# Kernel optimization log

Hardware: AMD Instinct MI355X
Metric: run time of the kernel (lower is better)

## Reference

```python
import jax, jax.numpy as jnp
import numpy as np
import math

D_MODEL = 1024
NUM_HEADS = 16
D_K = D_MODEL // NUM_HEADS
B, T = 2, 2048


def setup_inputs() -> dict:
    key = jax.random.key(0)
    ks = jax.random.split(key, 9)
    s = 1.0 / math.sqrt(D_MODEL)
    inp = {
        'x': jax.random.normal(ks[0], (B, T, D_MODEL), dtype=jnp.float32),
        'mask': jnp.tril(jnp.ones((1, 1, T, T), dtype=jnp.int32)),
        'Wq': jax.random.uniform(ks[1], (D_MODEL, D_MODEL), jnp.float32, -s, s),
        'bq': jax.random.uniform(ks[2], (D_MODEL,), jnp.float32, -s, s),
        'Wk': jax.random.uniform(ks[3], (D_MODEL, D_MODEL), jnp.float32, -s, s),
        'bk': jax.random.uniform(ks[4], (D_MODEL,), jnp.float32, -s, s),
        'Wv': jax.random.uniform(ks[5], (D_MODEL, D_MODEL), jnp.float32, -s, s),
        'bv': jax.random.uniform(ks[6], (D_MODEL,), jnp.float32, -s, s),
        'Wo': jax.random.uniform(ks[7], (D_MODEL, D_MODEL), jnp.float32, -s, s),
        'bo': jax.random.uniform(ks[8], (D_MODEL,), jnp.float32, -s, s),
    }
    return inp


def reference(x, mask, Wq, bq, Wk, bk, Wv, bv, Wo, bo):
    Bsz, Tlen, C = x.shape
    # projections; torch Linear computes x @ W.T + b, here W stored as (in,out)-like square so use x @ W + b with W meaning W.T
    q = (x @ Wq + bq).reshape(Bsz, Tlen, NUM_HEADS, D_K).transpose(0, 2, 1, 3)
    k = (x @ Wk + bk).reshape(Bsz, Tlen, NUM_HEADS, D_K).transpose(0, 2, 1, 3)
    v = (x @ Wv + bv).reshape(Bsz, Tlen, NUM_HEADS, D_K).transpose(0, 2, 1, 3)
    scores = jnp.einsum('bhqd,bhkd->bhqk', q, k) / math.sqrt(D_K)  # (B,H,T,T)
    scores = jnp.where(mask == 0, -jnp.inf, scores)
    attn = jax.nn.softmax(scores, axis=-1)
    out = jnp.einsum('bhqk,bhkd->bhqd', attn, v)
    out = out.transpose(0, 2, 1, 3).reshape(Bsz, Tlen, C)
    return out @ Wo + bo
```

## Files before the change

### kernel.cpp

```cpp
#include <hip/hip_runtime.h>
#include <math.h>

typedef unsigned short ushort_t;
typedef short short8 __attribute__((ext_vector_type(8)));
typedef float f32x4 __attribute__((ext_vector_type(4)));

#define DMODEL 1024
#define NHEADS 16
#define DKH    64
#define BATCH  2
#define SEQ    2048
#define BT     (BATCH * SEQ)

__device__ __forceinline__ ushort_t f2bf(float f) {
    union { float f; unsigned u; } a; a.f = f;
    return (ushort_t)((a.u + 0x7FFFu + ((a.u >> 16) & 1u)) >> 16);
}

__device__ __forceinline__ void async_copy16(const ushort_t* g, ushort_t* l) {
    __builtin_amdgcn_global_load_lds(
        (__attribute__((address_space(1))) void*)g,
        (__attribute__((address_space(3))) void*)l, 16, 0, 0);
}

__global__ __launch_bounds__(256) void cast_x_kernel(
    const float* __restrict__ x, ushort_t* __restrict__ xb)
{
    size_t i = ((size_t)blockIdx.x * 256 + threadIdx.x) * 8;
    float4 a = *(const float4*)(x + i);
    float4 b = *(const float4*)(x + i + 4);
    union { ushort_t u[8]; short8 v; } r;
    r.u[0] = f2bf(a.x); r.u[1] = f2bf(a.y); r.u[2] = f2bf(a.z); r.u[3] = f2bf(a.w);
    r.u[4] = f2bf(b.x); r.u[5] = f2bf(b.y); r.u[6] = f2bf(b.z); r.u[7] = f2bf(b.w);
    *(short8*)(xb + i) = r.v;
}

__global__ __launch_bounds__(256) void wtrans_kernel(
    const float* __restrict__ Wq, const float* __restrict__ Wk,
    const float* __restrict__ Wv, const float* __restrict__ Wo,
    ushort_t* __restrict__ WqT, ushort_t* __restrict__ WkT,
    ushort_t* __restrict__ WvT, ushort_t* __restrict__ WoT)
{
    const int z = blockIdx.z;
    const float* W = (z == 0) ? Wq : (z == 1) ? Wk : (z == 2) ? Wv : Wo;
    ushort_t*   WT = (z == 0) ? WqT : (z == 1) ? WkT : (z == 2) ? WvT : WoT;

    __shared__ ushort_t tile[64][72];
    const int k0 = blockIdx.x * 64, n0 = blockIdx.y * 64;
    const int tid = threadIdx.x;

    const int r  = tid >> 2;
    const int cb = (tid & 3) * 16;
#pragma unroll
    for (int u = 0; u < 4; ++u) {
        float4 v = *(const float4*)(W + (size_t)(k0 + r) * DMODEL + n0 + cb + u * 4);
        union { ushort_t u4[4]; unsigned long long ll; } p;
        p.u4[0] = f2bf(v.x); p.u4[1] = f2bf(v.y); p.u4[2] = f2bf(v.z); p.u4[3] = f2bf(v.w);
        *(unsigned long long*)&tile[r][cb + u * 4] = p.ll;
    }
    __syncthreads();
    const int n  = tid >> 2;
    const int kb = (tid & 3) * 16;
#pragma unroll
    for (int half = 0; half < 2; ++half) {
        union { ushort_t u8[8]; short8 v; } p;
#pragma unroll
        for (int j = 0; j < 8; ++j) p.u8[j] = tile[kb + half * 8 + j][n];
        *(short8*)(WT + (size_t)(n0 + n) * DMODEL + k0 + kb + half * 8) = p.v;
    }
}

__device__ __forceinline__ void gemm_mainloop(
    const ushort_t* __restrict__ A, const ushort_t* __restrict__ B,
    int m0, int n0, ushort_t* At, ushort_t* Bt, f32x4 (&acc)[4][4])
{
    const int tid  = threadIdx.x;
    const int w    = tid >> 6, lane = tid & 63;
    const int l15  = lane & 15, quad = lane >> 4;
    const int wm   = w >> 1, wn = w & 1;
    const int srow = lane >> 3;
    const int scol = ((lane & 7) ^ srow) << 3;
    const int swz  = l15 & 7;

    for (int k0 = 0; k0 < DMODEL; k0 += 64) {
        __syncthreads();
#pragma unroll
        for (int c = 0; c < 4; ++c) {
            int chunk = w * 4 + c;
            async_copy16(A + (size_t)(m0 + chunk * 8 + srow) * DMODEL + k0 + scol,
                         At + chunk * 512);
            async_copy16(B + (size_t)(n0 + chunk * 8 + srow) * DMODEL + k0 + scol,
                         Bt + chunk * 512);
        }
        __syncthreads();
#pragma unroll
        for (int kk = 0; kk < 2; ++kk) {
            short8 af[4], bf[4];
#pragma unroll
            for (int t = 0; t < 4; ++t) {
                af[t] = *(const short8*)(At + (wm * 64 + t * 16 + l15) * 64 +
                                         (((kk * 4 + quad) ^ swz) << 3));
                bf[t] = *(const short8*)(Bt + (wn * 64 + t * 16 + l15) * 64 +
                                         (((kk * 4 + quad) ^ swz) << 3));
            }
#pragma unroll
            for (int mt = 0; mt < 4; ++mt)
#pragma unroll
                for (int nt = 0; nt < 4; ++nt)
                    acc[mt][nt] = __builtin_amdgcn_mfma_f32_16x16x32_bf16(
                        af[mt], bf[nt], acc[mt][nt], 0, 0, 0);
        }
    }
}

__device__ __forceinline__ void gemm_mainloop_n64(
    const ushort_t* __restrict__ A, const ushort_t* __restrict__ B,
    int m0, int n0, ushort_t* At, ushort_t* Bt, f32x4 (&acc)[4][2])
{
    const int tid  = threadIdx.x;
    const int w    = tid >> 6, lane = tid & 63;
    const int l15  = lane & 15, quad = lane >> 4;
    const int wm   = w >> 1, wn = w & 1;
    const int srow = lane >> 3;
    const int scol = ((lane & 7) ^ srow) << 3;
    const int swz  = l15 & 7;

    for (int k0 = 0; k0 < DMODEL; k0 += 64) {
        __syncthreads();
#pragma unroll
        for (int c = 0; c < 4; ++c) {
            int chunk = w * 4 + c;
            async_copy16(A + (size_t)(m0 + chunk * 8 + srow) * DMODEL + k0 + scol,
                         At + chunk * 512);
        }
#pragma unroll
        for (int c = 0; c < 2; ++c) {
            int chunk = w * 2 + c;
            async_copy16(B + (size_t)(n0 + chunk * 8 + srow) * DMODEL + k0 + scol,
                         Bt + chunk * 512);
        }
        __syncthreads();
#pragma unroll
        for (int kk = 0; kk < 2; ++kk) {
            short8 af[4], bf[2];
#pragma unroll
            for (int t = 0; t < 4; ++t)
                af[t] = *(const short8*)(At + (wm * 64 + t * 16 + l15) * 64 +
                                         (((kk * 4 + quad) ^ swz) << 3));
#pragma unroll
            for (int t = 0; t < 2; ++t)
                bf[t] = *(const short8*)(Bt + (wn * 32 + t * 16 + l15) * 64 +
                                         (((kk * 4 + quad) ^ swz) << 3));
#pragma unroll
            for (int mt = 0; mt < 4; ++mt)
#pragma unroll
                for (int nt = 0; nt < 2; ++nt)
                    acc[mt][nt] = __builtin_amdgcn_mfma_f32_16x16x32_bf16(
                        af[mt], bf[nt], acc[mt][nt], 0, 0, 0);
        }
    }
}

__global__ __launch_bounds__(256) void qkv_gemm(
    const ushort_t* __restrict__ xb,
    const ushort_t* __restrict__ WqT, const ushort_t* __restrict__ WkT,
    const ushort_t* __restrict__ WvT,
    const float* __restrict__ bq, const float* __restrict__ bk,
    const float* __restrict__ bv,
    ushort_t* __restrict__ Qb, ushort_t* __restrict__ Kb, ushort_t* __restrict__ VTo)
{
    const int z = blockIdx.z;
    const ushort_t* WT = (z == 0) ? WqT : (z == 1) ? WkT : WvT;
    const float* bias  = (z == 0) ? bq : (z == 1) ? bk : bv;

    __shared__ ushort_t At[128 * 64];
    __shared__ ushort_t Bt[128 * 64];
    const int m0 = blockIdx.x * 128, n0 = blockIdx.y * 128;

    f32x4 zero = {0.f, 0.f, 0.f, 0.f};
    f32x4 acc[4][4];
#pragma unroll
    for (int i = 0; i < 4; ++i)
#pragma unroll
        for (int j = 0; j < 4; ++j) acc[i][j] = zero;

    gemm_mainloop(xb, WT, m0, n0, At, Bt, acc);

    const int tid = threadIdx.x, w = tid >> 6, lane = tid & 63;
    const int l15 = lane & 15, quad = lane >> 4;
    const int wm = w >> 1, wn = w & 1;

    float bcol[4];
#pragma unroll
    for (int nt = 0; nt < 4; ++nt) bcol[nt] = bias[n0 + wn * 64 + nt * 16 + l15];

    if (z == 2) {
#pragma unroll
        for (int mt = 0; mt < 4; ++mt) {
            int row0 = m0 + wm * 64 + mt * 16 + quad * 4;
            int b = row0 >> 11, t = row0 & (SEQ - 1);
            int tb = t & ~63;
            int idxp = ((mt & 1) << 2) | (quad << 3) | ((mt >> 1) << 5);
#pragma unroll
            for (int nt = 0; nt < 4; ++nt) {
                int col = n0 + wn * 64 + nt * 16 + l15;
                int h = col >> 6, d = col & 63;
                union { ushort_t u4[4]; unsigned long long ll; } pk;
#pragma unroll
                for (int reg = 0; reg < 4; ++reg)
                    pk.u4[reg] = f2bf(acc[mt][nt][reg] + bcol[nt]);
                *(unsigned long long*)(VTo +
                    ((size_t)(b * NHEADS + h) * DKH + d) * SEQ + tb + idxp) = pk.ll;
            }
        }
    } else {
        ushort_t* out = (z == 0) ? Qb : Kb;
#pragma unroll
        for (int mt = 0; mt < 4; ++mt)
#pragma unroll
            for (int reg = 0; reg < 4; ++reg) {
                int row = m0 + wm * 64 + mt * 16 + quad * 4 + reg;
                int b = row >> 11, t = row & (SEQ - 1);
#pragma unroll
                for (int nt = 0; nt < 4; ++nt) {
                    int col = n0 + wn * 64 + nt * 16 + l15;
                    int h = col >> 6, d = col & 63;
                    out[((((size_t)b * NHEADS + h) * SEQ + t) << 6) + d] =
                        f2bf(acc[mt][nt][reg] + bcol[nt]);
                }
            }
    }
}

__global__ __launch_bounds__(256) void attn_kernel(
    const ushort_t* __restrict__ Qb, const ushort_t* __restrict__ Kb,
    const ushort_t* __restrict__ VT, ushort_t* __restrict__ AO)
{
    const int bi = blockIdx.x;
    const int bh = bi >> 4;
    const int b  = bh >> 4, h = bh & 15;
    const int qq = bi & 15;
    const int tid = threadIdx.x, w = tid >> 6, lane = tid & 63;
    const int l15 = lane & 15, quad = lane >> 4;

    __shared__ ushort_t Kt[2][64 * 64];
    __shared__ ushort_t Vt[2][64 * 64];

    const ushort_t* Kbase = Kb + (((size_t)bh * SEQ) << 6);
    const ushort_t* Vbase = VT + (size_t)bh * DKH * SEQ;

    const int srow = lane >> 3;
    const int schx = (lane & 7) ^ srow;
    const int swz  = l15 & 7;
    const f32x4 zero = {0.f, 0.f, 0.f, 0.f};
    const float cexp = 0.18033688011112042f;

    for (int job = 0; job < 2; ++job) {
        const int qt = job ? (31 - qq) : qq;
        const int q0 = qt * 64;
        const int nk = qt + 1;

        short8 qa[2];
#pragma unroll
        for (int ks = 0; ks < 2; ++ks)
            qa[ks] = *(const short8*)(
                Qb + (((size_t)bh * SEQ + q0 + w * 16 + l15) << 6) + ks * 32 + quad * 8);

        float l_i = 0.f;
        f32x4 o[4];
#pragma unroll
        for (int dt = 0; dt < 4; ++dt) o[dt] = zero;

#pragma unroll
        for (int c = 0; c < 2; ++c) {
            int chunk = w * 2 + c;
            async_copy16(Kbase + (((size_t)(chunk * 8 + srow)) << 6) + schx * 8,
                         &Kt[0][chunk * 512]);
            async_copy16(Vbase + (size_t)(chunk * 8 + srow) * SEQ + schx * 8,
                         &Vt[0][chunk * 512]);
        }
        __syncthreads();

        for (int kt = 0; kt < nk; ++kt) {
            const int buf = kt & 1;
            if (kt + 1 < nk) {
                const int kt0n = (kt + 1) * 64;
#pragma unroll
                for (int c = 0; c < 2; ++c) {
                    int chunk = w * 2 + c;
                    async_copy16(Kbase + (((size_t)(kt0n + chunk * 8 + srow)) << 6) + schx * 8,
                                 &Kt[buf ^ 1][chunk * 512]);
                    async_copy16(Vbase + (size_t)(chunk * 8 + srow) * SEQ + kt0n + schx * 8,
                                 &Vt[buf ^ 1][chunk * 512]);
                }
            }

            short8 kf[4][2], vf[2][4];
#pragma unroll
            for (int kt_i = 0; kt_i < 4; ++kt_i)
#pragma unroll
                for (int ks = 0; ks < 2; ++ks)
                    kf[kt_i][ks] = *(const short8*)&Kt[buf][(kt_i * 16 + l15) * 64 +
                                                            (((ks * 4 + quad) ^ swz) << 3)];
#pragma unroll
            for (int g = 0; g < 2; ++g)
#pragma unroll
                for (int dt = 0; dt < 4; ++dt)
                    vf[g][dt] = *(const short8*)&Vt[buf][(dt * 16 + l15) * 64 +
                                                         ((((g << 2) | quad) ^ swz) << 3)];

            f32x4 sc[4];
#pragma unroll
            for (int kt_i = 0; kt_i < 4; ++kt_i) sc[kt_i] = zero;
#pragma unroll
            for (int ks = 0; ks < 2; ++ks)
#pragma unroll
                for (int kt_i = 0; kt_i < 4; ++kt_i)
                    sc[kt_i] = __builtin_amdgcn_mfma_f32_16x16x32_bf16(
                        kf[kt_i][ks], qa[ks], sc[kt_i], 0, 0, 0);

            const bool domask = (kt == qt);
            const int qabs = q0 + w * 16 + l15;
            unsigned pka[4], pkb[4];
            float lp = 0.f;
#pragma unroll
            for (int kt_i = 0; kt_i < 4; ++kt_i) {
                unsigned u[4];
#pragma unroll
                for (int r = 0; r < 4; ++r) {
                    float p = exp2f(cexp * sc[kt_i][r]);
                    if (domask && (kt * 64 + kt_i * 16 + quad * 4 + r) > qabs) p = 0.f;
                    u[r] = __float_as_uint(p) & 0xFFFF0000u;
                    lp += __uint_as_float(u[r]);
                }
                pka[kt_i] = (u[0] >> 16) | u[1];
                pkb[kt_i] = (u[2] >> 16) | u[3];
            }
            l_i += lp;

#pragma unroll
            for (int g = 0; g < 2; ++g) {
                union { unsigned u[4]; short8 v; } pf;
                pf.u[0] = pka[2 * g];
                pf.u[1] = pkb[2 * g];
                pf.u[2] = pka[2 * g + 1];
                pf.u[3] = pkb[2 * g + 1];
#pragma unroll
                for (int dt = 0; dt < 4; ++dt)
                    o[dt] = __builtin_amdgcn_mfma_f32_16x16x32_bf16(
                        pf.v, vf[g][dt], o[dt], 0, 0, 0);
            }

            __syncthreads();
        }

        float l = l_i;
        l += __shfl_xor(l, 16);
        l += __shfl_xor(l, 32);
        float inv = 1.0f / l;
#pragma unroll
        for (int r = 0; r < 4; ++r) {
            float invr = __shfl(inv, quad * 4 + r, 16);
            int t = q0 + w * 16 + quad * 4 + r;
#pragma unroll
            for (int dt = 0; dt < 4; ++dt)
                AO[((size_t)b * SEQ + t) * DMODEL + h * 64 + dt * 16 + l15] =
                    f2bf(o[dt][r] * invr);
        }
    }
}

__global__ __launch_bounds__(256) void out_gemm(
    const ushort_t* __restrict__ AO, const ushort_t* __restrict__ WoT,
    const float* __restrict__ bo, float* __restrict__ out)
{
    __shared__ ushort_t At[128 * 64];
    __shared__ ushort_t Bt[64 * 64];
    const int m0 = blockIdx.x * 128, n0 = blockIdx.y * 64;

    f32x4 zero = {0.f, 0.f, 0.f, 0.f};
    f32x4 acc[4][2];
#pragma unroll
    for (int i = 0; i < 4; ++i)
#pragma unroll
        for (int j = 0; j < 2; ++j) acc[i][j] = zero;

    gemm_mainloop_n64(AO, WoT, m0, n0, At, Bt, acc);

    const int tid = threadIdx.x, w = tid >> 6, lane = tid & 63;
    const int l15 = lane & 15, quad = lane >> 4;
    const int wm = w >> 1, wn = w & 1;

    float bcol[2];
#pragma unroll
    for (int nt = 0; nt < 2; ++nt) bcol[nt] = bo[n0 + wn * 32 + nt * 16 + l15];

#pragma unroll
    for (int mt = 0; mt < 4; ++mt)
#pragma unroll
        for (int reg = 0; reg < 4; ++reg) {
            int row = m0 + wm * 64 + mt * 16 + quad * 4 + reg;
#pragma unroll
            for (int nt = 0; nt < 2; ++nt) {
                int col = n0 + wn * 32 + nt * 16 + l15;
                out[(size_t)row * DMODEL + col] = acc[mt][nt][reg] + bcol[nt];
            }
        }
}

extern "C" void kernel_launch(void* const* d_in, const int* in_sizes, int n_in,
                              void* d_out, int out_size, void* d_ws, size_t ws_size,
                              hipStream_t stream)
{
    const float* x  = (const float*)d_in[0];
    const float* Wq = (const float*)d_in[2];
    const float* bq = (const float*)d_in[3];
    const float* Wk = (const float*)d_in[4];
    const float* bk = (const float*)d_in[5];
    const float* Wv = (const float*)d_in[6];
    const float* bv = (const float*)d_in[7];
    const float* Wo = (const float*)d_in[8];
    const float* bo = (const float*)d_in[9];
    float* out = (float*)d_out;

    ushort_t* ws = (ushort_t*)d_ws;
    size_t off = 0;
    ushort_t* xb  = ws + off; off += (size_t)BT * DMODEL;
    ushort_t* WqT = ws + off; off += (size_t)DMODEL * DMODEL;
    ushort_t* WkT = ws + off; off += (size_t)DMODEL * DMODEL;
    ushort_t* WvT = ws + off; off += (size_t)DMODEL * DMODEL;
    ushort_t* WoT = ws + off; off += (size_t)DMODEL * DMODEL;
    ushort_t* Qb  = ws + off; off += (size_t)BT * DMODEL;
    ushort_t* Kb  = ws + off; off += (size_t)BT * DMODEL;
    ushort_t* VTb = ws + off; off += (size_t)BT * DMODEL;
    ushort_t* AOb = ws + off; off += (size_t)BT * DMODEL;

    cast_x_kernel<<<(BT * DMODEL) / (256 * 8), 256, 0, stream>>>(x, xb);
    wtrans_kernel<<<dim3(16, 16, 4), 256, 0, stream>>>(
        Wq, Wk, Wv, Wo, WqT, WkT, WvT, WoT);
    qkv_gemm<<<dim3(BT / 128, DMODEL / 128, 3), 256, 0, stream>>>(
        xb, WqT, WkT, WvT, bq, bk, bv, Qb, Kb, VTb);
    attn_kernel<<<dim3(SEQ / 64 * NHEADS * BATCH / 2), 256, 0, stream>>>(
        Qb, Kb, VTb, AOb);
    out_gemm<<<dim3(BT / 128, DMODEL / 64), 256, 0, stream>>>(
        AOb, WoT, bo, out);
}
```

Measured before the change: 211.1 us.

## Double-buffer LDS tiles in projection GEMMs with K-step 32 prefetch

Replaces the single-buffered K=64 mainloops of the QKV and output projection GEMMs with double-buffered K=32 loops. The next tile is prefetched asynchronously into the alternate LDS buffer while MFMAs run on the current one, leaving one barrier per iteration instead of two. It also switches to a rotation-based LDS swizzle that fits the 32-wide rows. The trade is twice as many loop iterations with smaller loads, and correctness depends on the async global-to-LDS copies having landed by the single barrier.

```diff
diff --git a/kernel.cpp b/kernel.cpp
--- a/kernel.cpp
+++ b/kernel.cpp
@@ -70,7 +70,7 @@
     }
 }
 
-__device__ __forceinline__ void gemm_mainloop(
+__device__ __forceinline__ void gemm_dbuf_128(
     const ushort_t* __restrict__ A, const ushort_t* __restrict__ B,
     int m0, int n0, ushort_t* At, ushort_t* Bt, f32x4 (&acc)[4][4])
 {
@@ -78,42 +78,51 @@
     const int w    = tid >> 6, lane = tid & 63;
     const int l15  = lane & 15, quad = lane >> 4;
     const int wm   = w >> 1, wn = w & 1;
-    const int srow = lane >> 3;
-    const int scol = ((lane & 7) ^ srow) << 3;
-    const int swz  = l15 & 7;
-
-    for (int k0 = 0; k0 < DMODEL; k0 += 64) {
+    const int rw   = lane >> 2;
+    const int sco  = (((lane & 3) - (lane >> 4)) & 3) << 3;
+
+    const ushort_t* Arow = A + (size_t)(m0 + rw) * DMODEL + sco;
+    const ushort_t* Brow = B + (size_t)(n0 + rw) * DMODEL + sco;
+
+#pragma unroll
+    for (int c = 0; c < 2; ++c) {
+        int ch = w * 2 + c;
+        async_copy16(Arow + (size_t)ch * 16 * DMODEL, At + ch * 512);
+        async_copy16(Brow + (size_t)ch * 16 * DMODEL, Bt + ch * 512);
+    }
+    __syncthreads();
+
+    for (int kt = 0; kt < DMODEL / 32; ++kt) {
+        const int cur = (kt & 1) << 12;
+        if (kt + 1 < DMODEL / 32) {
+            const int nxt = cur ^ 4096;
+            const int k0 = (kt + 1) * 32;
+#pragma unroll
+            for (int c = 0; c < 2; ++c) {
+                int ch = w * 2 + c;
+                async_copy16(Arow + (size_t)ch * 16 * DMODEL + k0, At + nxt + ch * 512);
+                async_copy16(Brow + (size_t)ch * 16 * DMODEL + k0, Bt + nxt + ch * 512);
+            }
+        }
+        short8 af[4], bf[4];
+#pragma unroll
+        for (int t = 0; t < 4; ++t) {
+            int ra = wm * 64 + t * 16 + l15;
+            int rb = wn * 64 + t * 16 + l15;
+            af[t] = *(const short8*)(At + cur + ra * 32 + (((quad + (ra >> 2)) & 3) << 3));
+            bf[t] = *(const short8*)(Bt + cur + rb * 32 + (((quad + (rb >> 2)) & 3) << 3));
+        }
+#pragma unroll
+        for (int mt = 0; mt < 4; ++mt)
+#pragma unroll
+            for (int nt = 0; nt < 4; ++nt)
+                acc[mt][nt] = __builtin_amdgcn_mfma_f32_16x16x32_bf16(
+                    af[mt], bf[nt], acc[mt][nt], 0, 0, 0);
         __syncthreads();
-#pragma unroll
-        for (int c = 0; c < 4; ++c) {
-            int chunk = w * 4 + c;
-            async_copy16(A + (size_t)(m0 + chunk * 8 + srow) * DMODEL + k0 + scol,
-                         At + chunk * 512);
-            async_copy16(B + (size_t)(n0 + chunk * 8 + srow) * DMODEL + k0 + scol,
-                         Bt + chunk * 512);
-        }
-        __syncthreads();
-#pragma unroll
-        for (int kk = 0; kk < 2; ++kk) {
-            short8 af[4], bf[4];
-#pragma unroll
-            for (int t = 0; t < 4; ++t) {
-                af[t] = *(const short8*)(At + (wm * 64 + t * 16 + l15) * 64 +
-                                         (((kk * 4 + quad) ^ swz) << 3));
-                bf[t] = *(const short8*)(Bt + (wn * 64 + t * 16 + l15) * 64 +
-                                         (((kk * 4 + quad) ^ swz) << 3));
-            }
-#pragma unroll
-            for (int mt = 0; mt < 4; ++mt)
-#pragma unroll
-                for (int nt = 0; nt < 4; ++nt)
-                    acc[mt][nt] = __builtin_amdgcn_mfma_f32_16x16x32_bf16(
-                        af[mt], bf[nt], acc[mt][nt], 0, 0, 0);
-        }
-    }
-}
-
-__device__ __forceinline__ void gemm_mainloop_n64(
+    }
+}
+
+__device__ __forceinline__ void gemm_dbuf_n64(
     const ushort_t* __restrict__ A, const ushort_t* __restrict__ B,
     int m0, int n0, ushort_t* At, ushort_t* Bt, f32x4 (&acc)[4][2])
 {
@@ -121,43 +130,52 @@
     const int w    = tid >> 6, lane = tid & 63;
     const int l15  = lane & 15, quad = lane >> 4;
     const int wm   = w >> 1, wn = w & 1;
-    const int srow = lane >> 3;
-    const int scol = ((lane & 7) ^ srow) << 3;
-    const int swz  = l15 & 7;
-
-    for (int k0 = 0; k0 < DMODEL; k0 += 64) {
+    const int rw   = lane >> 2;
+    const int sco  = (((lane & 3) - (lane >> 4)) & 3) << 3;
+
+    const ushort_t* Arow = A + (size_t)(m0 + rw) * DMODEL + sco;
+    const ushort_t* Brow = B + (size_t)(n0 + rw) * DMODEL + sco;
+
+#pragma unroll
+    for (int c = 0; c < 2; ++c) {
+        int ch = w * 2 + c;
+        async_copy16(Arow + (size_t)ch * 16 * DMODEL, At + ch * 512);
+    }
+    async_copy16(Brow + (size_t)w * 16 * DMODEL, Bt + w * 512);
+    __syncthreads();
+
+    for (int kt = 0; kt < DMODEL / 32; ++kt) {
+        const int curA = (kt & 1) << 12;
+        const int curB = (kt & 1) << 11;
+        if (kt + 1 < DMODEL / 32) {
+            const int k0 = (kt + 1) * 32;
+#pragma unroll
+            for (int c = 0; c < 2; ++c) {
+                int ch = w * 2 + c;
+                async_copy16(Arow + (size_t)ch * 16 * DMODEL + k0,
+                             At + (curA ^ 4096) + ch * 512);
+            }
+            async_copy16(Brow + (size_t)w * 16 * DMODEL + k0,
+                         Bt + (curB ^ 2048) + w * 512);
+        }
+        short8 af[4], bf[2];
+#pragma unroll
+        for (int t = 0; t < 4; ++t) {
+            int ra = wm * 64 + t * 16 + l15;
+            af[t] = *(const short8*)(At + curA + ra * 32 + (((quad + (ra >> 2)) & 3) << 3));
+        }
+#pragma unroll
+        for (int t = 0; t < 2; ++t) {
+            int rb = wn * 32 + t * 16 + l15;
+            bf[t] = *(const short8*)(Bt + curB + rb * 32 + (((quad + (rb >> 2)) & 3) << 3));
+        }
+#pragma unroll
+        for (int mt = 0; mt < 4; ++mt)
+#pragma unroll
+            for (int nt = 0; nt < 2; ++nt)
+                acc[mt][nt] = __builtin_amdgcn_mfma_f32_16x16x32_bf16(
+                    af[mt], bf[nt], acc[mt][nt], 0, 0, 0);
         __syncthreads();
-#pragma unroll
-        for (int c = 0; c < 4; ++c) {
-            int chunk = w * 4 + c;
-            async_copy16(A + (size_t)(m0 + chunk * 8 + srow) * DMODEL + k0 + scol,
-                         At + chunk * 512);
-        }
-#pragma unroll
-        for (int c = 0; c < 2; ++c) {
-            int chunk = w * 2 + c;
-            async_copy16(B + (size_t)(n0 + chunk * 8 + srow) * DMODEL + k0 + scol,
-                         Bt + chunk * 512);
-        }
-        __syncthreads();
-#pragma unroll
-        for (int kk = 0; kk < 2; ++kk) {
-            short8 af[4], bf[2];
-#pragma unroll
-            for (int t = 0; t < 4; ++t)
-                af[t] = *(const short8*)(At + (wm * 64 + t * 16 + l15) * 64 +
-                                         (((kk * 4 + quad) ^ swz) << 3));
-#pragma unroll
-            for (int t = 0; t < 2; ++t)
-                bf[t] = *(const short8*)(Bt + (wn * 32 + t * 16 + l15) * 64 +
-                                         (((kk * 4 + quad) ^ swz) << 3));
-#pragma unroll
-            for (int mt = 0; mt < 4; ++mt)
-#pragma unroll
-                for (int nt = 0; nt < 2; ++nt)
-                    acc[mt][nt] = __builtin_amdgcn_mfma_f32_16x16x32_bf16(
-                        af[mt], bf[nt], acc[mt][nt], 0, 0, 0);
-        }
     }
 }
 
@@ -173,8 +191,8 @@
     const ushort_t* WT = (z == 0) ? WqT : (z == 1) ? WkT : WvT;
     const float* bias  = (z == 0) ? bq : (z == 1) ? bk : bv;
 
-    __shared__ ushort_t At[128 * 64];
-    __shared__ ushort_t Bt[128 * 64];
+    __shared__ ushort_t At[2 * 4096];
+    __shared__ ushort_t Bt[2 * 4096];
     const int m0 = blockIdx.x * 128, n0 = blockIdx.y * 128;
 
     f32x4 zero = {0.f, 0.f, 0.f, 0.f};
@@ -184,7 +202,7 @@
 #pragma unroll
         for (int j = 0; j < 4; ++j) acc[i][j] = zero;
 
-    gemm_mainloop(xb, WT, m0, n0, At, Bt, acc);
+    gemm_dbuf_128(xb, WT, m0, n0, At, Bt, acc);
 
     const int tid = threadIdx.x, w = tid >> 6, lane = tid & 63;
     const int l15 = lane & 15, quad = lane >> 4;
@@ -374,8 +392,8 @@
     const ushort_t* __restrict__ AO, const ushort_t* __restrict__ WoT,
     const float* __restrict__ bo, float* __restrict__ out)
 {
-    __shared__ ushort_t At[128 * 64];
-    __shared__ ushort_t Bt[64 * 64];
+    __shared__ ushort_t At[2 * 4096];
+    __shared__ ushort_t Bt[2 * 2048];
     const int m0 = blockIdx.x * 128, n0 = blockIdx.y * 64;
 
     f32x4 zero = {0.f, 0.f, 0.f, 0.f};
@@ -385,7 +403,7 @@
 #pragma unroll
         for (int j = 0; j < 2; ++j) acc[i][j] = zero;
 
-    gemm_mainloop_n64(AO, WoT, m0, n0, At, Bt, acc);
+    gemm_dbuf_n64(AO, WoT, m0, n0, At, Bt, acc);
 
     const int tid = threadIdx.x, w = tid >> 6, lane = tid & 63;
     const int l15 = lane & 15, quad = lane >> 4;
```

After: 225.5 us. +6.8%, slower.

## Double-buffer GEMM LDS tiles and reorder attention block-to-head mapping

Applied to the files above, without the earlier changes.

Both projection GEMM mainloops now use two LDS buffers: the next K-tile's async global-to-LDS copies are issued before the MFMA work on the current tile, with one barrier per iteration. The aim is to hide global load latency behind compute. This doubles shared memory per block (64KB for the QKV GEMM), which may cut occupancy. The attention kernel's block index mapping is also swapped so consecutive blocks cover different heads rather than q-tiles of the same head, changing scheduling and cache locality.

```diff
diff --git a/kernel.cpp b/kernel.cpp
--- a/kernel.cpp
+++ b/kernel.cpp
@@ -70,7 +70,7 @@
     }
 }
 
-__device__ __forceinline__ void gemm_mainloop(
+__device__ __forceinline__ void gemm_dbuf_128(
     const ushort_t* __restrict__ A, const ushort_t* __restrict__ B,
     int m0, int n0, ushort_t* At, ushort_t* Bt, f32x4 (&acc)[4][4])
 {
@@ -82,25 +82,38 @@
     const int scol = ((lane & 7) ^ srow) << 3;
     const int swz  = l15 & 7;
 
-    for (int k0 = 0; k0 < DMODEL; k0 += 64) {
-        __syncthreads();
-#pragma unroll
-        for (int c = 0; c < 4; ++c) {
-            int chunk = w * 4 + c;
-            async_copy16(A + (size_t)(m0 + chunk * 8 + srow) * DMODEL + k0 + scol,
-                         At + chunk * 512);
-            async_copy16(B + (size_t)(n0 + chunk * 8 + srow) * DMODEL + k0 + scol,
-                         Bt + chunk * 512);
-        }
-        __syncthreads();
+#pragma unroll
+    for (int c = 0; c < 4; ++c) {
+        int ch = w * 4 + c;
+        async_copy16(A + (size_t)(m0 + ch * 8 + srow) * DMODEL + scol, At + ch * 512);
+        async_copy16(B + (size_t)(n0 + ch * 8 + srow) * DMODEL + scol, Bt + ch * 512);
+    }
+    __syncthreads();
+
+    for (int kt = 0; kt < DMODEL / 64; ++kt) {
+        const int cur = (kt & 1) << 13;
+        if (kt + 1 < DMODEL / 64) {
+            const int nxt = cur ^ 8192;
+            const int k0 = (kt + 1) * 64;
+#pragma unroll
+            for (int c = 0; c < 4; ++c) {
+                int ch = w * 4 + c;
+                async_copy16(A + (size_t)(m0 + ch * 8 + srow) * DMODEL + k0 + scol,
+                             At + nxt + ch * 512);
+                async_copy16(B + (size_t)(n0 + ch * 8 + srow) * DMODEL + k0 + scol,
+                             Bt + nxt + ch * 512);
+            }
+        }
 #pragma unroll
         for (int kk = 0; kk < 2; ++kk) {
             short8 af[4], bf[4];
 #pragma unroll
             for (int t = 0; t < 4; ++t) {
-                af[t] = *(const short8*)(At + (wm * 64 + t * 16 + l15) * 64 +
+                int ra = wm * 64 + t * 16 + l15;
+                int rb = wn * 64 + t * 16 + l15;
+                af[t] = *(const short8*)(At + cur + ra * 64 +
                                          (((kk * 4 + quad) ^ swz) << 3));
-                bf[t] = *(const short8*)(Bt + (wn * 64 + t * 16 + l15) * 64 +
+                bf[t] = *(const short8*)(Bt + cur + rb * 64 +
                                          (((kk * 4 + quad) ^ swz) << 3));
             }
 #pragma unroll
@@ -110,10 +123,11 @@
                     acc[mt][nt] = __builtin_amdgcn_mfma_f32_16x16x32_bf16(
                         af[mt], bf[nt], acc[mt][nt], 0, 0, 0);
         }
-    }
-}
-
-__device__ __forceinline__ void gemm_mainloop_n64(
+        __syncthreads();
+    }
+}
+
+__device__ __forceinline__ void gemm_dbuf_n64(
     const ushort_t* __restrict__ A, const ushort_t* __restrict__ B,
     int m0, int n0, ushort_t* At, ushort_t* Bt, f32x4 (&acc)[4][2])
 {
@@ -125,32 +139,51 @@
     const int scol = ((lane & 7) ^ srow) << 3;
     const int swz  = l15 & 7;
 
-    for (int k0 = 0; k0 < DMODEL; k0 += 64) {
-        __syncthreads();
-#pragma unroll
-        for (int c = 0; c < 4; ++c) {
-            int chunk = w * 4 + c;
-            async_copy16(A + (size_t)(m0 + chunk * 8 + srow) * DMODEL + k0 + scol,
-                         At + chunk * 512);
-        }
-#pragma unroll
-        for (int c = 0; c < 2; ++c) {
-            int chunk = w * 2 + c;
-            async_copy16(B + (size_t)(n0 + chunk * 8 + srow) * DMODEL + k0 + scol,
-                         Bt + chunk * 512);
-        }
-        __syncthreads();
+#pragma unroll
+    for (int c = 0; c < 4; ++c) {
+        int ch = w * 4 + c;
+        async_copy16(A + (size_t)(m0 + ch * 8 + srow) * DMODEL + scol, At + ch * 512);
+    }
+#pragma unroll
+    for (int c = 0; c < 2; ++c) {
+        int ch = w * 2 + c;
+        async_copy16(B + (size_t)(n0 + ch * 8 + srow) * DMODEL + scol, Bt + ch * 512);
+    }
+    __syncthreads();
+
+    for (int kt = 0; kt < DMODEL / 64; ++kt) {
+        const int curA = (kt & 1) << 13;
+        const int curB = (kt & 1) << 12;
+        if (kt + 1 < DMODEL / 64) {
+            const int k0 = (kt + 1) * 64;
+#pragma unroll
+            for (int c = 0; c < 4; ++c) {
+                int ch = w * 4 + c;
+                async_copy16(A + (size_t)(m0 + ch * 8 + srow) * DMODEL + k0 + scol,
+                             At + (curA ^ 8192) + ch * 512);
+            }
+#pragma unroll
+            for (int c = 0; c < 2; ++c) {
+                int ch = w * 2 + c;
+                async_copy16(B + (size_t)(n0 + ch * 8 + srow) * DMODEL + k0 + scol,
+                             Bt + (curB ^ 4096) + ch * 512);
+            }
+        }
 #pragma unroll
         for (int kk = 0; kk < 2; ++kk) {
             short8 af[4], bf[2];
 #pragma unroll
-            for (int t = 0; t < 4; ++t)
-                af[t] = *(const short8*)(At + (wm * 64 + t * 16 + l15) * 64 +
+            for (int t = 0; t < 4; ++t) {
+                int ra = wm * 64 + t * 16 + l15;
+                af[t] = *(const short8*)(At + curA + ra * 64 +
                                          (((kk * 4 + quad) ^ swz) << 3));
-#pragma unroll
-            for (int t = 0; t < 2; ++t)
-                bf[t] = *(const short8*)(Bt + (wn * 32 + t * 16 + l15) * 64 +
+            }
+#pragma unroll
+            for (int t = 0; t < 2; ++t) {
+                int rb = wn * 32 + t * 16 + l15;
+                bf[t] = *(const short8*)(Bt + curB + rb * 64 +
                                          (((kk * 4 + quad) ^ swz) << 3));
+            }
 #pragma unroll
             for (int mt = 0; mt < 4; ++mt)
 #pragma unroll
@@ -158,6 +191,7 @@
                     acc[mt][nt] = __builtin_amdgcn_mfma_f32_16x16x32_bf16(
                         af[mt], bf[nt], acc[mt][nt], 0, 0, 0);
         }
+        __syncthreads();
     }
 }
 
@@ -173,8 +207,8 @@
     const ushort_t* WT = (z == 0) ? WqT : (z == 1) ? WkT : WvT;
     const float* bias  = (z == 0) ? bq : (z == 1) ? bk : bv;
 
-    __shared__ ushort_t At[128 * 64];
-    __shared__ ushort_t Bt[128 * 64];
+    __shared__ ushort_t At[2 * 8192];
+    __shared__ ushort_t Bt[2 * 8192];
     const int m0 = blockIdx.x * 128, n0 = blockIdx.y * 128;
 
     f32x4 zero = {0.f, 0.f, 0.f, 0.f};
@@ -184,7 +218,7 @@
 #pragma unroll
         for (int j = 0; j < 4; ++j) acc[i][j] = zero;
 
-    gemm_mainloop(xb, WT, m0, n0, At, Bt, acc);
+    gemm_dbuf_128(xb, WT, m0, n0, At, Bt, acc);
 
     const int tid = threadIdx.x, w = tid >> 6, lane = tid & 63;
     const int l15 = lane & 15, quad = lane >> 4;
@@ -237,9 +271,9 @@
     const ushort_t* __restrict__ VT, ushort_t* __restrict__ AO)
 {
     const int bi = blockIdx.x;
-    const int bh = bi >> 4;
+    const int bh = bi & 31;
     const int b  = bh >> 4, h = bh & 15;
-    const int qq = bi & 15;
+    const int qq = bi >> 5;
     const int tid = threadIdx.x, w = tid >> 6, lane = tid & 63;
     const int l15 = lane & 15, quad = lane >> 4;
 
@@ -374,8 +408,8 @@
     const ushort_t* __restrict__ AO, const ushort_t* __restrict__ WoT,
     const float* __restrict__ bo, float* __restrict__ out)
 {
-    __shared__ ushort_t At[128 * 64];
-    __shared__ ushort_t Bt[64 * 64];
+    __shared__ ushort_t At[2 * 8192];
+    __shared__ ushort_t Bt[2 * 4096];
     const int m0 = blockIdx.x * 128, n0 = blockIdx.y * 64;
 
     f32x4 zero = {0.f, 0.f, 0.f, 0.f};
@@ -385,7 +419,7 @@
 #pragma unroll
         for (int j = 0; j < 2; ++j) acc[i][j] = zero;
 
-    gemm_mainloop_n64(AO, WoT, m0, n0, At, Bt, acc);
+    gemm_dbuf_n64(AO, WoT, m0, n0, At, Bt, acc);
 
     const int tid = threadIdx.x, w = tid >> 6, lane = tid & 63;
     const int l15 = lane & 15, quad = lane >> 4;
```

Measured after the change: 204.5 us. 1.03x faster.
